# Performance work log

Hardware: AMD Instinct MI355X
Metric: run time of the kernel (lower is better)

## Reference

```python
import jax, jax.numpy as jnp
import numpy as np

B, N, C, D = 32, 4096, 16, 256

def setup_inputs() -> dict:
    key = jax.random.key(0)
    k1, k2 = jax.random.split(key)
    r_tensor = jax.random.uniform(k1, (B, N, C), dtype=jnp.float32)
    v_tensor = jax.random.normal(k2, (B, N, D), dtype=jnp.float32)
    return {"r_tensor": r_tensor, "v_tensor": v_tensor}

def reference(r_tensor, v_tensor):
    n = r_tensor.shape[1]
    mask_belong = r_tensor >= 0.5  # (B,N,C)
    # mean over N of v[:, :, None, :] * mask[..., None]  ==  mask^T @ v / N, no (B,N,C,D) intermediate
    interest_category_mean = jnp.einsum(
        'bnc,bnd->bcd', mask_belong.astype(v_tensor.dtype), v_tensor) / n  # (B,C,D)
    mask_all_below = jnp.logical_not(mask_belong).all(axis=2)  # (B,N)
    interest_special_mean = jnp.einsum(
        'bn,bnd->bd', mask_all_below.astype(v_tensor.dtype), v_tensor) / n  # (B,D)
    v_fusion = jnp.concatenate(
        [interest_category_mean, interest_special_mean[:, None, :]], axis=1)  # (B,C+1,D)
    v_fusion = jnp.where(jnp.isnan(v_fusion), jnp.zeros((), v_fusion.dtype), v_fusion)
    return v_fusion
```

## Files before the change

kernel.cpp:

```cpp
#include <hip/hip_runtime.h>

#define B_ 32
#define N_ 4096
#define C_ 16
#define D_ 256
#define NSPLIT 64
#define ROWS 64
#define RPS  32
#define NG   8

__global__ __launch_bounds__(256, 8)
void tensor_fusion_kernel(const float* __restrict__ r,
                          const float* __restrict__ v,
                          float* __restrict__ out) {
    const int b     = blockIdx.x >> 6;
    const int chunk = blockIdx.x & (NSPLIT - 1);
    const int tid   = threadIdx.x;
    const int wave  = tid >> 6;
    const int lane  = tid & 63;
    const int sub   = wave >> 1;
    const int half  = wave & 1;
    const int d2    = half * 128 + (lane << 1);

    const float* __restrict__ rb = r + (size_t)b * N_ * C_;
    const float* __restrict__ vp = v + (size_t)b * N_ * D_;
    const float scale = 1.0f / (float)N_;
    float* __restrict__ ob = out + (size_t)b * 17 * D_;

    float2 acc[16];
#pragma unroll
    for (int c = 0; c < 16; ++c) acc[c] = make_float2(0.f, 0.f);

    const int base = chunk * ROWS + sub * RPS;
    const float* __restrict__ rptr = rb + (size_t)base * C_ + lane;
    const float* __restrict__ vptr = vp + (size_t)base * D_ + d2;

    float  rv, rv_n;
    float2 v0, v1, v2, v3, n0, n1, n2, n3;

#define LOADG(off, RV, A, Bq, Cq, Dq)                          \
    {                                                          \
        RV = rptr[(size_t)(off) * C_];                         \
        const float* _vn = vptr + (size_t)(off) * D_;          \
        A  = *(const float2*)(_vn + 0 * D_);                   \
        Bq = *(const float2*)(_vn + 1 * D_);                   \
        Cq = *(const float2*)(_vn + 2 * D_);                   \
        Dq = *(const float2*)(_vn + 3 * D_);                   \
    }

#define ACCROW(VV, MASK)                                       \
    {                                                          \
        const unsigned _m = (MASK);                            \
        _Pragma("unroll")                                      \
        for (int c = 0; c < 16; ++c) {                         \
            const float m = (_m & (1u << c)) ? 1.0f : 0.0f;    \
            acc[c].x += (VV).x * m;                            \
            acc[c].y += (VV).y * m;                            \
        }                                                      \
        if (_m == 0u) {        \
            atomicAdd(&ob[16 * D_ + d2 + 0], (VV).x * scale);  \
            atomicAdd(&ob[16 * D_ + d2 + 1], (VV).y * scale);  \
        }                                                      \
    }

    LOADG(0, rv, v0, v1, v2, v3);

#pragma unroll
    for (int g = 0; g < NG; ++g) {
        if (g + 1 < NG) LOADG((g + 1) * 4, rv_n, n0, n1, n2, n3);

        const unsigned long long bal = __ballot(rv >= 0.5f);
        ACCROW(v0, (unsigned)(bal       ) & 0xFFFFu);
        ACCROW(v1, (unsigned)(bal >> 16 ) & 0xFFFFu);
        ACCROW(v2, (unsigned)(bal >> 32 ) & 0xFFFFu);
        ACCROW(v3, (unsigned)(bal >> 48 ) & 0xFFFFu);

        if (g + 1 < NG) { rv = rv_n; v0 = n0; v1 = n1; v2 = n2; v3 = n3; }
    }

    __shared__ float2 lds2[16 * 128];
    const int li = half * 64 + lane;
    if (sub == 0) {
#pragma unroll
        for (int c = 0; c < 16; ++c) lds2[c * 128 + li] = acc[c];
    }
    __syncthreads();
    if (sub == 1) {
#pragma unroll
        for (int c = 0; c < 16; ++c) {
            float2 t = lds2[c * 128 + li];
            t.x += acc[c].x; t.y += acc[c].y;
            lds2[c * 128 + li] = t;
        }
    }
    __syncthreads();

    const float* lf = (const float*)lds2;
#pragma unroll
    for (int c = 0; c < 16; ++c) {
        atomicAdd(&ob[c * D_ + tid], lf[c * 256 + tid] * scale);
    }
}

extern "C" void kernel_launch(void* const* d_in, const int* in_sizes, int n_in,
                              void* d_out, int out_size, void* d_ws, size_t ws_size,
                              hipStream_t stream) {
    const float* r = (const float*)d_in[0];
    const float* v = (const float*)d_in[1];
    float* out = (float*)d_out;

    hipMemsetAsync(out, 0, (size_t)out_size * sizeof(float), stream);

    dim3 grid(B_ * NSPLIT);
    tensor_fusion_kernel<<<grid, 256, 0, stream>>>(r, v, out);
}
```

Before: 236.3 us.

## Replace atomics with two-stage workspace reduction and float4 per-wave row split

The single kernel that used float atomics into a memset output becomes two kernels. Stage one has each of four waves process a quarter of the chunk's rows with float4 loads across all 256 columns. It keeps the all-below special row in a 17th register accumulator instead of issuing per-row atomics, reduces the waves through LDS, and writes partial sums to a workspace. Stage two sums the 64 partials per output element and scales them, which removes the memset and all atomics at the cost of an extra launch, extra workspace traffic and higher register pressure.

```diff
diff --git a/kernel.cpp b/kernel.cpp
--- a/kernel.cpp
+++ b/kernel.cpp
@@ -5,47 +5,43 @@
 #define C_ 16
 #define D_ 256
 #define NSPLIT 64
-#define ROWS 64
-#define RPS  32
-#define NG   8
+#define ROWS (N_ / NSPLIT)
+#define RPW  (ROWS / 4)
+#define NG   (RPW / 4)
 
-__global__ __launch_bounds__(256, 8)
-void tensor_fusion_kernel(const float* __restrict__ r,
-                          const float* __restrict__ v,
-                          float* __restrict__ out) {
+__global__ __launch_bounds__(256, 4)
+void tf_stage1(const float* __restrict__ r,
+               const float* __restrict__ v,
+               float* __restrict__ ws) {
     const int b     = blockIdx.x >> 6;
     const int chunk = blockIdx.x & (NSPLIT - 1);
     const int tid   = threadIdx.x;
     const int wave  = tid >> 6;
     const int lane  = tid & 63;
-    const int sub   = wave >> 1;
-    const int half  = wave & 1;
-    const int d2    = half * 128 + (lane << 1);
+    const int d4    = lane << 2;
 
     const float* __restrict__ rb = r + (size_t)b * N_ * C_;
     const float* __restrict__ vp = v + (size_t)b * N_ * D_;
-    const float scale = 1.0f / (float)N_;
-    float* __restrict__ ob = out + (size_t)b * 17 * D_;
 
-    float2 acc[16];
+    float4 acc[17];
 #pragma unroll
-    for (int c = 0; c < 16; ++c) acc[c] = make_float2(0.f, 0.f);
+    for (int c = 0; c < 17; ++c) acc[c] = make_float4(0.f, 0.f, 0.f, 0.f);
 
-    const int base = chunk * ROWS + sub * RPS;
+    const int base = chunk * ROWS + wave * RPW;
     const float* __restrict__ rptr = rb + (size_t)base * C_ + lane;
-    const float* __restrict__ vptr = vp + (size_t)base * D_ + d2;
+    const float* __restrict__ vptr = vp + (size_t)base * D_ + d4;
 
     float  rv, rv_n;
-    float2 v0, v1, v2, v3, n0, n1, n2, n3;
+    float4 v0, v1, v2, v3, n0, n1, n2, n3;
 
 #define LOADG(off, RV, A, Bq, Cq, Dq)                          \
     {                                                          \
         RV = rptr[(size_t)(off) * C_];                         \
         const float* _vn = vptr + (size_t)(off) * D_;          \
-        A  = *(const float2*)(_vn + 0 * D_);                   \
-        Bq = *(const float2*)(_vn + 1 * D_);                   \
-        Cq = *(const float2*)(_vn + 2 * D_);                   \
-        Dq = *(const float2*)(_vn + 3 * D_);                   \
+        A  = *(const float4*)(_vn + 0 * D_);                   \
+        Bq = *(const float4*)(_vn + 1 * D_);                   \
+        Cq = *(const float4*)(_vn + 2 * D_);                   \
+        Dq = *(const float4*)(_vn + 3 * D_);                   \
     }
 
 #define ACCROW(VV, MASK)                                       \
@@ -56,10 +52,12 @@
             const float m = (_m & (1u << c)) ? 1.0f : 0.0f;    \
             acc[c].x += (VV).x * m;                            \
             acc[c].y += (VV).y * m;                            \
+            acc[c].z += (VV).z * m;                            \
+            acc[c].w += (VV).w * m;                            \
         }                                                      \
-        if (_m == 0u) {        \
-            atomicAdd(&ob[16 * D_ + d2 + 0], (VV).x * scale);  \
-            atomicAdd(&ob[16 * D_ + d2 + 1], (VV).y * scale);  \
+        if (_m == 0u) {         \
+            acc[16].x += (VV).x; acc[16].y += (VV).y;          \
+            acc[16].z += (VV).z; acc[16].w += (VV).w;          \
         }                                                      \
     }
 
@@ -78,28 +76,46 @@
         if (g + 1 < NG) { rv = rv_n; v0 = n0; v1 = n1; v2 = n2; v3 = n3; }
     }
 
-    __shared__ float2 lds2[16 * 128];
-    const int li = half * 64 + lane;
-    if (sub == 0) {
+    __shared__ float4 lds4[17 * 64];
+    if (wave == 0) {
 #pragma unroll
-        for (int c = 0; c < 16; ++c) lds2[c * 128 + li] = acc[c];
+        for (int c = 0; c < 17; ++c) lds4[c * 64 + lane] = acc[c];
     }
     __syncthreads();
-    if (sub == 1) {
+    for (int w = 1; w < 4; ++w) {
+        if (wave == w) {
 #pragma unroll
-        for (int c = 0; c < 16; ++c) {
-            float2 t = lds2[c * 128 + li];
-            t.x += acc[c].x; t.y += acc[c].y;
-            lds2[c * 128 + li] = t;
+            for (int c = 0; c < 17; ++c) {
+                float4 t = lds4[c * 64 + lane];
+                t.x += acc[c].x; t.y += acc[c].y;
+                t.z += acc[c].z; t.w += acc[c].w;
+                lds4[c * 64 + lane] = t;
+            }
         }
+        __syncthreads();
     }
-    __syncthreads();
 
-    const float* lf = (const float*)lds2;
+    float* __restrict__ wsb = ws + (size_t)blockIdx.x * 17 * D_;
+    const float* lf = (const float*)lds4;
 #pragma unroll
-    for (int c = 0; c < 16; ++c) {
-        atomicAdd(&ob[c * D_ + tid], lf[c * 256 + tid] * scale);
+    for (int c = 0; c < 17; ++c) {
+        wsb[c * D_ + tid] = lf[c * 256 + tid];
     }
+}
+
+__global__ __launch_bounds__(256, 8)
+void tf_stage2(const float* __restrict__ ws, float* __restrict__ out) {
+    const int b = blockIdx.x / 17;
+    const int j = blockIdx.x % 17;
+    const int d = threadIdx.x;
+
+    const float* __restrict__ p =
+        ws + ((size_t)b * NSPLIT * 17 + j) * D_ + d;
+    float s = 0.0f;
+#pragma unroll 8
+    for (int k = 0; k < NSPLIT; ++k) s += p[(size_t)k * 17 * D_];
+
+    out[((size_t)b * 17 + j) * D_ + d] = s * (1.0f / (float)N_);
 }
 
 extern "C" void kernel_launch(void* const* d_in, const int* in_sizes, int n_in,
@@ -108,9 +124,8 @@
     const float* r = (const float*)d_in[0];
     const float* v = (const float*)d_in[1];
     float* out = (float*)d_out;
+    float* ws  = (float*)d_ws;
 
-    hipMemsetAsync(out, 0, (size_t)out_size * sizeof(float), stream);
-
-    dim3 grid(B_ * NSPLIT);
-    tensor_fusion_kernel<<<grid, 256, 0, stream>>>(r, v, out);
+    tf_stage1<<<dim3(B_ * NSPLIT), 256, 0, stream>>>(r, v, ws);
+    tf_stage2<<<dim3(B_ * 17), 256, 0, stream>>>(ws, out);
 }
```

Result: faster. 208.3 us (-11.8%).
